# Kernel tuning notes

Measured on AMD Instinct MI355X. Metric: run time of the kernel, lower is better.

## Reference

```python
import jax, jax.numpy as jnp
import numpy as np

DIM = 1024
HEAD_SIZE = 128
B, N = 4, 4096

def setup_inputs() -> dict:
    key = jax.random.key(0)
    kx, kq, kk, kv = jax.random.split(key, 4)
    s = (1.0 / DIM) ** 0.5  # ~ torch Linear init scale
    return {
        "x": jax.random.normal(kx, (B, N, DIM), dtype=jnp.float32),
        "Wq": jax.random.uniform(kq, (HEAD_SIZE, DIM), dtype=jnp.float32, minval=-s, maxval=s),
        "Wk": jax.random.uniform(kk, (HEAD_SIZE, DIM), dtype=jnp.float32, minval=-s, maxval=s),
        "Wv": jax.random.uniform(kv, (HEAD_SIZE, DIM), dtype=jnp.float32, minval=-s, maxval=s),
    }

def reference(x, Wq, Wk, Wv):
    # x: [B, N, dim]; W*: [head_size, dim] (torch Linear convention y = x @ W.T)
    q = jnp.einsum('bnd,hd->bnh', x, Wq)
    k = jnp.einsum('bnd,hd->bnh', x, Wk)
    v = jnp.einsum('bnd,hd->bnh', x, Wv)
    scale = DIM ** (-0.5)  # NOTE: original scales by dim**-0.5, not head_size
    scores = jnp.einsum('bnh,bmh->bnm', q, k) * scale  # [B, N, N]
    weights = jax.nn.softmax(scores, axis=-1)
    context = jnp.einsum('bnm,bmh->bnh', weights, v)  # [B, N, head_size]
    return context
```

## Files before the change

kernel.cpp:

```cpp
#include <hip/hip_runtime.h>

using bf16x8   = __attribute__((ext_vector_type(8))) __bf16;
using f32x4    = __attribute__((ext_vector_type(4))) float;
using f32x16   = __attribute__((ext_vector_type(16))) float;
using floatv4  = __attribute__((ext_vector_type(4))) float;
using ushortv4 = __attribute__((ext_vector_type(4))) unsigned short;
using ushortv8 = __attribute__((ext_vector_type(8))) unsigned short;
using uintv4   = __attribute__((ext_vector_type(4))) unsigned int;

#define N_SEQ 4096
#define N_B   4
#define DIMK  1024
#define HS    128
#define ROWS  (N_B * N_SEQ)
#define KVB   32
#define TT    (N_SEQ / KVB)

__device__ __forceinline__ unsigned short f2bf(float f) {
    unsigned u = __builtin_bit_cast(unsigned, f);
    u += 0x7FFFu + ((u >> 16) & 1u);
    return (unsigned short)(u >> 16);
}

__device__ __forceinline__ unsigned cvtpk(float lo, float hi) {
    unsigned r;
    asm("v_cvt_pk_bf16_f32 %0, %1, %2" : "=v"(r) : "v"(lo), "v"(hi));
    return r;
}

__device__ __forceinline__ void gload16(const unsigned short* g, unsigned short* l) {
    __builtin_amdgcn_global_load_lds(
        (const __attribute__((address_space(1))) unsigned int*)g,
        (__attribute__((address_space(3))) unsigned int*)l, 16, 0, 0);
}

__global__ __launch_bounds__(256) void cast_kernel(
    const float* __restrict__ X,
    const float* __restrict__ Wq,
    const float* __restrict__ Wk,
    const float* __restrict__ Wv,
    unsigned short* __restrict__ Xb,
    unsigned short* __restrict__ Wb)
{
    const int blk = blockIdx.x;
    const float* src;
    unsigned short* dst;
    size_t off;
    if (blk < 8192) {
        src = X; dst = Xb; off = (size_t)blk * 2048;
    } else {
        int wblk = blk - 8192;
        int z = wblk >> 6;
        src = (z == 0) ? Wq : (z == 1) ? Wk : Wv;
        dst = Wb + (size_t)z * (HS * DIMK);
        off = (size_t)(wblk & 63) * 2048;
    }
    size_t i = off + (size_t)threadIdx.x * 8;
    floatv4 a = *reinterpret_cast<const floatv4*>(src + i);
    floatv4 b = *reinterpret_cast<const floatv4*>(src + i + 4);
    ushortv8 o = { f2bf(a.x), f2bf(a.y), f2bf(a.z), f2bf(a.w),
                   f2bf(b.x), f2bf(b.y), f2bf(b.z), f2bf(b.w) };
    *reinterpret_cast<ushortv8*>(dst + i) = o;
}

__global__ __launch_bounds__(256, 3) void proj_kernel(
    const unsigned short* __restrict__ Xb,
    const unsigned short* __restrict__ Wb,
    unsigned short* __restrict__ Qb,
    unsigned short* __restrict__ Kb,
    unsigned short* __restrict__ Vt)
{
    const int z = blockIdx.y;
    const unsigned short* __restrict__ Wz = Wb + (size_t)z * (HS * DIMK);
    const int row0 = blockIdx.x * 64;
    __shared__ unsigned short smem[2 * 64 * 64 + 2 * 128 * 64];
    unsigned short* Xs0 = smem;
    unsigned short* Ws0 = smem + 2 * 64 * 64;
    const int tid = threadIdx.x;
    const int wv = tid >> 6, lane = tid & 63;
    const int lr = lane & 15, lg = lane >> 4;

    f32x4 acc[4][2] = {};

    auto stage = [&](int buf, int k0) {
        #pragma unroll
        for (int i = 0; i < 2; ++i) {
            int g = wv * 2 + i;
            int r = g * 8 + (lane >> 3);
            int sp = (lane & 7) ^ (r & 7);
            gload16(Xb + (size_t)(row0 + r) * DIMK + k0 + sp * 8,
                    Xs0 + buf * (64 * 64) + g * 8 * 64);
        }
        #pragma unroll
        for (int i = 0; i < 4; ++i) {
            int g = wv * 4 + i;
            int r = g * 8 + (lane >> 3);
            int sp = (lane & 7) ^ (r & 7);
            gload16(Wz + (size_t)r * DIMK + k0 + sp * 8,
                    Ws0 + buf * (128 * 64) + g * 8 * 64);
        }
    };

    stage(0, 0);
    __syncthreads();
    for (int ks = 0; ks < DIMK / 64; ++ks) {
        const int cur = ks & 1;
        if (ks < DIMK / 64 - 1) stage(cur ^ 1, (ks + 1) * 64);
        const unsigned short* Xc = Xs0 + cur * (64 * 64);
        const unsigned short* Wc = Ws0 + cur * (128 * 64);
        bf16x8 af[4][2], bfr[2][2];
        #pragma unroll
        for (int mi = 0; mi < 4; ++mi)
            #pragma unroll
            for (int kk = 0; kk < 2; ++kk)
                af[mi][kk] = *reinterpret_cast<const bf16x8*>(
                    &Xc[(mi * 16 + lr) * 64 + (((kk * 4 + lg) ^ (lr & 7)) * 8)]);
        #pragma unroll
        for (int ni = 0; ni < 2; ++ni)
            #pragma unroll
            for (int kk = 0; kk < 2; ++kk)
                bfr[ni][kk] = *reinterpret_cast<const bf16x8*>(
                    &Wc[(wv * 32 + ni * 16 + lr) * 64 + (((kk * 4 + lg) ^ (lr & 7)) * 8)]);
        #pragma unroll
        for (int kk = 0; kk < 2; ++kk)
            #pragma unroll
            for (int mi = 0; mi < 4; ++mi)
                #pragma unroll
                for (int ni = 0; ni < 2; ++ni)
                    acc[mi][ni] = __builtin_amdgcn_mfma_f32_16x16x32_bf16(
                        af[mi][kk], bfr[ni][kk], acc[mi][ni], 0, 0, 0);
        __syncthreads();
    }

    if (z < 2) {
        unsigned short* O = (z == 0) ? Qb : Kb;
        const float qs = (z == 0) ? 0.045084220027780106f : 1.0f;
        #pragma unroll
        for (int mi = 0; mi < 4; ++mi) {
            int rowb = row0 + mi * 16 + lg * 4;
            #pragma unroll
            for (int ni = 0; ni < 2; ++ni) {
                int col = wv * 32 + ni * 16 + lr;
                #pragma unroll
                for (int r = 0; r < 4; ++r)
                    O[(size_t)(rowb + r) * HS + col] = f2bf(acc[mi][ni][r] * qs);
            }
        }
    } else {
        unsigned short* Cs = smem;
        #pragma unroll
        for (int mi = 0; mi < 4; ++mi)
            #pragma unroll
            for (int ni = 0; ni < 2; ++ni)
                #pragma unroll
                for (int r = 0; r < 4; ++r)
                    Cs[(mi * 16 + lg * 4 + r) * 132 + wv * 32 + ni * 16 + lr] = f2bf(acc[mi][ni][r]);
        __syncthreads();
        const int b  = row0 >> 12;
        const int n0 = row0 & (N_SEQ - 1);
        #pragma unroll
        for (int i = 0; i < 4; ++i) {
            int idx = tid + i * 256;
            int d = idx >> 3, c8 = idx & 7;
            ushortv8 v;
            #pragma unroll
            for (int j = 0; j < 8; ++j)
                v[j] = Cs[(c8 * 8 + j) * 132 + d];
            *reinterpret_cast<ushortv8*>(Vt + (size_t)b * HS * N_SEQ + (size_t)d * N_SEQ + n0 + c8 * 8) = v;
        }
    }
}

__global__ __launch_bounds__(256, 3) void attn_kernel(
    const unsigned short* __restrict__ Qb,
    const unsigned short* __restrict__ Kb,
    const unsigned short* __restrict__ Vt,
    unsigned short* __restrict__ part,
    float* __restrict__ plsum,
    int S)
{
    const int qblk  = blockIdx.x;
    const int split = blockIdx.y;
    const int tid = threadIdx.x;
    const int wv = tid >> 6, lane = tid & 63;
    const int l31 = lane & 31, h = lane >> 5;
    const int b    = qblk >> 5;
    const int row0 = (qblk & 31) * 128 + wv * 32;

    __shared__ unsigned short Ks[3][KVB * 128];
    __shared__ unsigned short Vs[3][128 * KVB];

    bf16x8 qf[8];
    {
        const unsigned short* qp = Qb + ((size_t)b * N_SEQ + row0 + l31) * HS + h * 8;
        #pragma unroll
        for (int kk = 0; kk < 8; ++kk)
            qf[kk] = *reinterpret_cast<const bf16x8*>(qp + kk * 16);
    }

    const int base = TT / S, rem = TT % S;
    const int nt = base + (split < rem ? 1 : 0);
    const int kv_begin = (split * base + (split < rem ? split : rem)) * KVB;

    const unsigned short* Kbb = Kb + (size_t)b * N_SEQ * HS;
    const unsigned short* Vbb = Vt + (size_t)b * HS * N_SEQ;

    auto stage = [&](int buf, int kv0) {
        #pragma unroll
        for (int i = 0; i < 2; ++i) {
            int g = wv * 2 + i;
            int r = g * 4 + (lane >> 4);
            int sp = (lane & 15) ^ (r & 7);
            gload16(Kbb + (size_t)(kv0 + r) * HS + sp * 8, &Ks[buf][g * 4 * 128]);
        }
        #pragma unroll
        for (int i = 0; i < 2; ++i) {
            int g = wv * 2 + i;
            int r = g * 16 + (lane >> 2);
            int sp = (lane & 3) ^ ((r >> 1) & 3);
            gload16(Vbb + (size_t)r * N_SEQ + kv0 + sp * 8, &Vs[buf][g * 16 * KVB]);
        }
    };

    f32x16 ctx[4] = {};
    f32x16 lacc = {};
    const ushortv8 ones_u = {0x3F80,0x3F80,0x3F80,0x3F80,0x3F80,0x3F80,0x3F80,0x3F80};
    const bf16x8 onesf = __builtin_bit_cast(bf16x8, ones_u);

    stage(0, kv_begin);
    stage(1, kv_begin + KVB);
    int cur = 0, nxt = 2;
    for (int t = 0; t < nt; ++t) {
        if (t + 2 < nt) {
            asm volatile("s_waitcnt vmcnt(4)\n\ts_barrier" ::: "memory");
            stage(nxt, kv_begin + (t + 2) * KVB);
        } else if (t + 1 < nt) {
            asm volatile("s_waitcnt vmcnt(4)\n\ts_barrier" ::: "memory");
        } else {
            asm volatile("s_waitcnt vmcnt(0)\n\ts_barrier" ::: "memory");
        }

        f32x16 st = {};
        __builtin_amdgcn_s_setprio(1);
        #pragma unroll
        for (int kk = 0; kk < 8; ++kk) {
            bf16x8 kf = *reinterpret_cast<const bf16x8*>(
                &Ks[cur][l31 * 128 + (((kk * 2 + h) ^ (l31 & 7)) * 8)]);
            st = __builtin_amdgcn_mfma_f32_32x32x16_bf16(kf, qf[kk], st, 0, 0, 0);
        }
        __builtin_amdgcn_s_setprio(0);

        float p[16];
        #pragma unroll
        for (int r = 0; r < 16; ++r)
            p[r] = __builtin_amdgcn_exp2f(st[r]);

        bf16x8 pf[2];
        #pragma unroll
        for (int half = 0; half < 2; ++half) {
            unsigned a  = cvtpk(p[half*8 + 0], p[half*8 + 1]);
            unsigned bq = cvtpk(p[half*8 + 2], p[half*8 + 3]);
            unsigned c  = cvtpk(p[half*8 + 4], p[half*8 + 5]);
            unsigned d  = cvtpk(p[half*8 + 6], p[half*8 + 7]);
            asm("v_permlane32_swap_b32 %0, %1" : "+v"(a), "+v"(c));
            asm("v_permlane32_swap_b32 %0, %1" : "+v"(bq), "+v"(d));
            uintv4 w = { a, bq, c, d };
            pf[half] = __builtin_bit_cast(bf16x8, w);
        }

        __builtin_amdgcn_s_setprio(1);
        lacc = __builtin_amdgcn_mfma_f32_32x32x16_bf16(pf[0], onesf, lacc, 0, 0, 0);
        lacc = __builtin_amdgcn_mfma_f32_32x32x16_bf16(pf[1], onesf, lacc, 0, 0, 0);
        #pragma unroll
        for (int dt = 0; dt < 4; ++dt) {
            int d = dt * 32 + l31;
            bf16x8 vf0 = *reinterpret_cast<const bf16x8*>(
                &Vs[cur][d * KVB + (((0 + h) ^ ((d >> 1) & 3)) * 8)]);
            ctx[dt] = __builtin_amdgcn_mfma_f32_32x32x16_bf16(pf[0], vf0, ctx[dt], 0, 0, 0);
            bf16x8 vf1 = *reinterpret_cast<const bf16x8*>(
                &Vs[cur][d * KVB + (((2 + h) ^ ((d >> 1) & 3)) * 8)]);
            ctx[dt] = __builtin_amdgcn_mfma_f32_32x32x16_bf16(pf[1], vf1, ctx[dt], 0, 0, 0);
        }
        __builtin_amdgcn_s_setprio(0);

        cur = (cur == 2) ? 0 : cur + 1;
        nxt = (nxt == 2) ? 0 : nxt + 1;
    }

    const int qt = qblk * 4 + wv;
    unsigned short* pp = part + ((size_t)qt * S + split) * (32 * 128);
    #pragma unroll
    for (int rp = 0; rp < 4; ++rp)
        #pragma unroll
        for (int rq = 0; rq < 4; ++rq) {
            const int r = rp * 4 + rq;
            const int q = rq + 8 * rp + 4 * h;
            #pragma unroll
            for (int dt = 0; dt < 4; ++dt)
                pp[q * 128 + dt * 32 + l31] = (unsigned short)(cvtpk(ctx[dt][r], ctx[dt][r]) & 0xFFFFu);
        }
    if (l31 == 0) {
        float* pl = plsum + ((size_t)qt * S + split) * 32;
        #pragma unroll
        for (int rp = 0; rp < 4; ++rp)
            #pragma unroll
            for (int rq = 0; rq < 4; ++rq)
                pl[rq + 8 * rp + 4 * h] = lacc[rp * 4 + rq];
    }
}

__global__ __launch_bounds__(256) void reduce_kernel(
    const unsigned short* __restrict__ part,
    const float* __restrict__ plsum,
    float* __restrict__ out, int S)
{
    const int id = blockIdx.x * 256 + threadIdx.x;
    const int d4 = (id & 31) * 4;
    const int grow = id >> 5;
    const int qt = grow >> 5, q = grow & 31;
    f32x4 c = {0.f, 0.f, 0.f, 0.f};
    float l = 0.f;
    for (int s = 0; s < S; ++s) {
        ushortv4 pv = *reinterpret_cast<const ushortv4*>(
            &part[(((size_t)qt * S + s) * 32 + q) * 128 + d4]);
        #pragma unroll
        for (int j = 0; j < 4; ++j)
            c[j] += __builtin_bit_cast(float, (unsigned)pv[j] << 16);
        l += plsum[((size_t)qt * S + s) * 32 + q];
    }
    float inv = 1.0f / l;
    f32x4 o = { c[0]*inv, c[1]*inv, c[2]*inv, c[3]*inv };
    *reinterpret_cast<f32x4*>(&out[(size_t)grow * 128 + d4]) = o;
}

extern "C" void kernel_launch(void* const* d_in, const int* in_sizes, int n_in,
                              void* d_out, int out_size, void* d_ws, size_t ws_size,
                              hipStream_t stream) {
    const float* x  = (const float*)d_in[0];
    const float* wq = (const float*)d_in[1];
    const float* wk = (const float*)d_in[2];
    const float* wv = (const float*)d_in[3];

    unsigned short* Xb = (unsigned short*)d_ws;
    unsigned short* Wb = Xb + (size_t)ROWS * DIMK;
    unsigned short* Qb = Wb + (size_t)3 * HS * DIMK;
    unsigned short* Kb = Qb + (size_t)ROWS * HS;
    unsigned short* Vt = Kb + (size_t)ROWS * HS;
    float* plsum = (float*)(Vt + (size_t)N_B * HS * N_SEQ);
    unsigned short* part = (unsigned short*)d_ws;

    const size_t base = ((size_t)ROWS * DIMK + 3 * HS * DIMK + 3 * (size_t)ROWS * HS) * 2;
    int S;
    if      (ws_size >= base + 6 * (size_t)512 * 32 * 4) S = 6;
    else if (ws_size >= base + 4 * (size_t)512 * 32 * 4) S = 4;
    else if (ws_size >= base + 2 * (size_t)512 * 32 * 4) S = 2;
    else                                                 S = 1;

    cast_kernel<<<8192 + 192, 256, 0, stream>>>(x, wq, wk, wv, Xb, Wb);
    proj_kernel<<<dim3(256, 3), 256, 0, stream>>>(Xb, Wb, Qb, Kb, Vt);
    attn_kernel<<<dim3(128, S), 256, 0, stream>>>(Qb, Kb, Vt, part, plsum, S);
    reduce_kernel<<<(ROWS * HS) / 1024, 256, 0, stream>>>(part, plsum, (float*)d_out, S);
}
```

Baseline: 83.57 us.

## Fuse X bf16 cast into projection, split QK accumulators, scalar row-sum

Removes the separate fp32-to-bf16 cast pass over X. The projection kernel now loads fp32 X into registers, converts it, and writes it to swizzled LDS, so the bf16 copy of X is no longer written to and read back from global memory. The attention kernel splits the QK MFMA chain into two independent accumulators to shorten the dependency chain. It also replaces the two ones-vector MFMAs for the softmax denominator with scalar adds plus a cross-lane shuffle. The workspace layout now gives the partials their own region instead of aliasing the freed Xb buffer. The trade-off is that X loads in proj become synchronous register loads with a vmcnt(0) wait each k-step, which may reduce overlap, and 3x as many proj blocks (one per z) each re-read and convert fp32 X.

Measured after the change: 82.35 us. Within noise of the previous version (-1.5%).

```diff
diff --git a/kernel.cpp b/kernel.cpp
--- a/kernel.cpp
+++ b/kernel.cpp
@@ -34,28 +34,17 @@
         (__attribute__((address_space(3))) unsigned int*)l, 16, 0, 0);
 }
 
-__global__ __launch_bounds__(256) void cast_kernel(
-    const float* __restrict__ X,
+__global__ __launch_bounds__(256) void castw_kernel(
     const float* __restrict__ Wq,
     const float* __restrict__ Wk,
     const float* __restrict__ Wv,
-    unsigned short* __restrict__ Xb,
     unsigned short* __restrict__ Wb)
 {
     const int blk = blockIdx.x;
-    const float* src;
-    unsigned short* dst;
-    size_t off;
-    if (blk < 8192) {
-        src = X; dst = Xb; off = (size_t)blk * 2048;
-    } else {
-        int wblk = blk - 8192;
-        int z = wblk >> 6;
-        src = (z == 0) ? Wq : (z == 1) ? Wk : Wv;
-        dst = Wb + (size_t)z * (HS * DIMK);
-        off = (size_t)(wblk & 63) * 2048;
-    }
-    size_t i = off + (size_t)threadIdx.x * 8;
+    const int z = blk >> 6;
+    const float* src = (z == 0) ? Wq : (z == 1) ? Wk : Wv;
+    unsigned short* dst = Wb + (size_t)z * (HS * DIMK);
+    size_t i = (size_t)(blk & 63) * 2048 + (size_t)threadIdx.x * 8;
     floatv4 a = *reinterpret_cast<const floatv4*>(src + i);
     floatv4 b = *reinterpret_cast<const floatv4*>(src + i + 4);
     ushortv8 o = { f2bf(a.x), f2bf(a.y), f2bf(a.z), f2bf(a.w),
@@ -64,7 +53,7 @@
 }
 
 __global__ __launch_bounds__(256, 3) void proj_kernel(
-    const unsigned short* __restrict__ Xb,
+    const float* __restrict__ X,
     const unsigned short* __restrict__ Wb,
     unsigned short* __restrict__ Qb,
     unsigned short* __restrict__ Kb,
@@ -80,17 +69,28 @@
     const int wv = tid >> 6, lane = tid & 63;
     const int lr = lane & 15, lg = lane >> 4;
 
+    const int xrow = tid >> 2, xc = (tid & 3) * 16;
+    const float* xg = X + (size_t)(row0 + xrow) * DIMK + xc;
+    const int xs0 = (tid & 3) * 2;
+    floatv4 xr[4];
+
     f32x4 acc[4][2] = {};
 
-    auto stage = [&](int buf, int k0) {
-        #pragma unroll
-        for (int i = 0; i < 2; ++i) {
-            int g = wv * 2 + i;
-            int r = g * 8 + (lane >> 3);
-            int sp = (lane & 7) ^ (r & 7);
-            gload16(Xb + (size_t)(row0 + r) * DIMK + k0 + sp * 8,
-                    Xs0 + buf * (64 * 64) + g * 8 * 64);
-        }
+    auto loadX = [&](int k0) {
+        #pragma unroll
+        for (int i = 0; i < 4; ++i)
+            xr[i] = *reinterpret_cast<const floatv4*>(xg + k0 + i * 4);
+    };
+    auto writeX = [&](int buf) {
+        uintv4 w0 = { cvtpk(xr[0].x, xr[0].y), cvtpk(xr[0].z, xr[0].w),
+                      cvtpk(xr[1].x, xr[1].y), cvtpk(xr[1].z, xr[1].w) };
+        uintv4 w1 = { cvtpk(xr[2].x, xr[2].y), cvtpk(xr[2].z, xr[2].w),
+                      cvtpk(xr[3].x, xr[3].y), cvtpk(xr[3].z, xr[3].w) };
+        unsigned short* xb = Xs0 + buf * (64 * 64) + xrow * 64;
+        *reinterpret_cast<uintv4*>(&xb[((xs0 ^ (xrow & 7)) * 8)]) = w0;
+        *reinterpret_cast<uintv4*>(&xb[(((xs0 + 1) ^ (xrow & 7)) * 8)]) = w1;
+    };
+    auto stageW = [&](int buf, int k0) {
         #pragma unroll
         for (int i = 0; i < 4; ++i) {
             int g = wv * 4 + i;
@@ -101,11 +101,17 @@
         }
     };
 
-    stage(0, 0);
+    loadX(0);
+    stageW(0, 0);
+    asm volatile("s_waitcnt vmcnt(0)" ::: "memory");
+    writeX(0);
     __syncthreads();
+
     for (int ks = 0; ks < DIMK / 64; ++ks) {
         const int cur = ks & 1;
-        if (ks < DIMK / 64 - 1) stage(cur ^ 1, (ks + 1) * 64);
+        const bool more = (ks + 1 < DIMK / 64);
+        if (more) { loadX((ks + 1) * 64); stageW(cur ^ 1, (ks + 1) * 64); }
+
         const unsigned short* Xc = Xs0 + cur * (64 * 64);
         const unsigned short* Wc = Ws0 + cur * (128 * 64);
         bf16x8 af[4][2], bfr[2][2];
@@ -129,6 +135,11 @@
                 for (int ni = 0; ni < 2; ++ni)
                     acc[mi][ni] = __builtin_amdgcn_mfma_f32_16x16x32_bf16(
                         af[mi][kk], bfr[ni][kk], acc[mi][ni], 0, 0, 0);
+
+        if (more) {
+            asm volatile("s_waitcnt vmcnt(0)" ::: "memory");
+            writeX(cur ^ 1);
+        }
         __syncthreads();
     }
 
@@ -223,9 +234,7 @@
     };
 
     f32x16 ctx[4] = {};
-    f32x16 lacc = {};
-    const ushortv8 ones_u = {0x3F80,0x3F80,0x3F80,0x3F80,0x3F80,0x3F80,0x3F80,0x3F80};
-    const bf16x8 onesf = __builtin_bit_cast(bf16x8, ones_u);
+    float lsum = 0.f;
 
     stage(0, kv_begin);
     stage(1, kv_begin + KVB);
@@ -240,20 +249,31 @@
             asm volatile("s_waitcnt vmcnt(0)\n\ts_barrier" ::: "memory");
         }
 
-        f32x16 st = {};
+        f32x16 st0 = {}, st1 = {};
         __builtin_amdgcn_s_setprio(1);
         #pragma unroll
-        for (int kk = 0; kk < 8; ++kk) {
-            bf16x8 kf = *reinterpret_cast<const bf16x8*>(
+        for (int kk = 0; kk < 8; kk += 2) {
+            bf16x8 kf0 = *reinterpret_cast<const bf16x8*>(
                 &Ks[cur][l31 * 128 + (((kk * 2 + h) ^ (l31 & 7)) * 8)]);
-            st = __builtin_amdgcn_mfma_f32_32x32x16_bf16(kf, qf[kk], st, 0, 0, 0);
+            st0 = __builtin_amdgcn_mfma_f32_32x32x16_bf16(kf0, qf[kk], st0, 0, 0, 0);
+            bf16x8 kf1 = *reinterpret_cast<const bf16x8*>(
+                &Ks[cur][l31 * 128 + ((((kk + 1) * 2 + h) ^ (l31 & 7)) * 8)]);
+            st1 = __builtin_amdgcn_mfma_f32_32x32x16_bf16(kf1, qf[kk + 1], st1, 0, 0, 0);
         }
         __builtin_amdgcn_s_setprio(0);
 
         float p[16];
         #pragma unroll
         for (int r = 0; r < 16; ++r)
-            p[r] = __builtin_amdgcn_exp2f(st[r]);
+            p[r] = __builtin_amdgcn_exp2f(st0[r] + st1[r]);
+
+        {
+            float a0 = (p[0] + p[1])   + (p[2] + p[3]);
+            float a1 = (p[4] + p[5])   + (p[6] + p[7]);
+            float a2 = (p[8] + p[9])   + (p[10] + p[11]);
+            float a3 = (p[12] + p[13]) + (p[14] + p[15]);
+            lsum += (a0 + a1) + (a2 + a3);
+        }
 
         bf16x8 pf[2];
         #pragma unroll
@@ -269,8 +289,6 @@
         }
 
         __builtin_amdgcn_s_setprio(1);
-        lacc = __builtin_amdgcn_mfma_f32_32x32x16_bf16(pf[0], onesf, lacc, 0, 0, 0);
-        lacc = __builtin_amdgcn_mfma_f32_32x32x16_bf16(pf[1], onesf, lacc, 0, 0, 0);
         #pragma unroll
         for (int dt = 0; dt < 4; ++dt) {
             int d = dt * 32 + l31;
@@ -287,6 +305,8 @@
         nxt = (nxt == 2) ? 0 : nxt + 1;
     }
 
+    lsum += __shfl_xor(lsum, 32);
+
     const int qt = qblk * 4 + wv;
     unsigned short* pp = part + ((size_t)qt * S + split) * (32 * 128);
     #pragma unroll
@@ -299,14 +319,8 @@
             for (int dt = 0; dt < 4; ++dt)
                 pp[q * 128 + dt * 32 + l31] = (unsigned short)(cvtpk(ctx[dt][r], ctx[dt][r]) & 0xFFFFu);
         }
-    if (l31 == 0) {
-        float* pl = plsum + ((size_t)qt * S + split) * 32;
-        #pragma unroll
-        for (int rp = 0; rp < 4; ++rp)
-            #pragma unroll
-            for (int rq = 0; rq < 4; ++rq)
-                pl[rq + 8 * rp + 4 * h] = lacc[rp * 4 + rq];
-    }
+    if (h == 0)
+        plsum[((size_t)qt * S + split) * 32 + l31] = lsum;
 }
 
 __global__ __launch_bounds__(256) void reduce_kernel(
@@ -341,23 +355,25 @@
     const float* wk = (const float*)d_in[2];
     const float* wv = (const float*)d_in[3];
 
-    unsigned short* Xb = (unsigned short*)d_ws;
-    unsigned short* Wb = Xb + (size_t)ROWS * DIMK;
+    unsigned short* Wb = (unsigned short*)d_ws;
     unsigned short* Qb = Wb + (size_t)3 * HS * DIMK;
     unsigned short* Kb = Qb + (size_t)ROWS * HS;
     unsigned short* Vt = Kb + (size_t)ROWS * HS;
     float* plsum = (float*)(Vt + (size_t)N_B * HS * N_SEQ);
-    unsigned short* part = (unsigned short*)d_ws;
-
-    const size_t base = ((size_t)ROWS * DIMK + 3 * HS * DIMK + 3 * (size_t)ROWS * HS) * 2;
+
+    const size_t fixed = (size_t)3 * HS * DIMK * 2 + (size_t)3 * ROWS * HS * 2;
+    const size_t per_split = (size_t)512 * 32 * 4 + (size_t)512 * 32 * 128 * 2;
+
     int S;
-    if      (ws_size >= base + 6 * (size_t)512 * 32 * 4) S = 6;
-    else if (ws_size >= base + 4 * (size_t)512 * 32 * 4) S = 4;
-    else if (ws_size >= base + 2 * (size_t)512 * 32 * 4) S = 2;
-    else                                                 S = 1;
-
-    cast_kernel<<<8192 + 192, 256, 0, stream>>>(x, wq, wk, wv, Xb, Wb);
-    proj_kernel<<<dim3(256, 3), 256, 0, stream>>>(Xb, Wb, Qb, Kb, Vt);
+    if      (ws_size >= fixed + 6 * per_split) S = 6;
+    else if (ws_size >= fixed + 4 * per_split) S = 4;
+    else if (ws_size >= fixed + 2 * per_split) S = 2;
+    else                                       S = 1;
+
+    unsigned short* part = (unsigned short*)(plsum + (size_t)512 * S * 32);
+
+    castw_kernel<<<192, 256, 0, stream>>>(wq, wk, wv, Wb);
+    proj_kernel<<<dim3(256, 3), 256, 0, stream>>>(x, Wb, Qb, Kb, Vt);
     attn_kernel<<<dim3(128, S), 256, 0, stream>>>(Qb, Kb, Vt, part, plsum, S);
     reduce_kernel<<<(ROWS * HS) / 1024, 256, 0, stream>>>(part, plsum, (float*)d_out, S);
 }
```
